# Kernel optimization log

Hardware: AMD Instinct MI355X
Metric: run time of the kernel (lower is better)

The kernel has to match this reference:

```python
import jax, jax.numpy as jnp
import numpy as np

B, S, D = 4, 2048, 1024
H, HD = 16, 64
L = 512          # kv latent dim (MLA compression)
E, TOPK, F = 8, 2, 2048  # MoE experts / top-k / expert hidden
EPS = 1e-6


def rmsnorm(x, g):
    return x * jax.lax.rsqrt(jnp.mean(x * x, axis=-1, keepdims=True) + EPS) * g


def setup_inputs() -> dict:
    key = jax.random.key(0)
    ks = jax.random.split(key, 16)
    std = 0.02
    inp = {
        "prev_hidden": jax.random.normal(ks[0], (B, S, D), jnp.float32),
        "future_token_embed": jax.random.normal(ks[1], (B, S, D), jnp.float32),
        "w_combine": jax.random.normal(ks[2], (2 * D, D), jnp.float32) * std,
        "g1": jnp.ones((D,), jnp.float32),
        "g2": jnp.ones((D,), jnp.float32),
        "g_attn": jnp.ones((D,), jnp.float32),
        "g_mlp": jnp.ones((D,), jnp.float32),
        "wq": jax.random.normal(ks[3], (D, D), jnp.float32) * std,
        "w_dkv": jax.random.normal(ks[4], (D, L), jnp.float32) * std,
        "w_uk": jax.random.normal(ks[5], (L, D), jnp.float32) * std,
        "w_uv": jax.random.normal(ks[6], (L, D), jnp.float32) * std,
        "wo": jax.random.normal(ks[7], (D, D), jnp.float32) * std,
        "w_gate": jax.random.normal(ks[8], (D, E), jnp.float32) * std,
        "w1": jax.random.normal(ks[9], (E, D, F), jnp.float32) * std,
        "w3": jax.random.normal(ks[10], (E, D, F), jnp.float32) * std,
        "w2": jax.random.normal(ks[11], (E, F, D), jnp.float32) * std,
    }
    return inp


def mla_attention(x, wq, w_dkv, w_uk, w_uv, wo):
    # Multi-head latent attention: KV compressed through latent dim L.
    q = (x @ wq).reshape(B, S, H, HD)
    c = x @ w_dkv                       # [B,S,L] latent
    k = (c @ w_uk).reshape(B, S, H, HD)
    v = (c @ w_uv).reshape(B, S, H, HD)
    scores = jnp.einsum("bqhd,bkhd->bhqk", q, k) / jnp.sqrt(jnp.float32(HD))
    causal = jnp.tril(jnp.ones((S, S), bool))
    scores = jnp.where(causal, scores, jnp.float32(-1e9))
    attn = jax.nn.softmax(scores, axis=-1)
    out = jnp.einsum("bhqk,bkhd->bqhd", attn, v).reshape(B, S, D)
    return out @ wo


def moe(x, w_gate, w1, w3, w2):
    t = x.reshape(-1, D)                          # [T,D]
    probs = jax.nn.softmax(t @ w_gate, axis=-1)   # [T,E]
    vals, idx = jax.lax.top_k(probs, TOPK)        # [T,K]
    vals = vals / jnp.sum(vals, axis=-1, keepdims=True)
    gates = jnp.sum(vals[:, :, None] * jax.nn.one_hot(idx, E, dtype=x.dtype), axis=1)  # [T,E]
    out = jnp.zeros_like(t)
    for e in range(E):  # fixed small expert loop (structurally distinct weights)
        h = jax.nn.silu(t @ w1[e]) * (t @ w3[e])
        out = out + gates[:, e:e + 1] * (h @ w2[e])
    return out.reshape(x.shape)


def reference(prev_hidden, future_token_embed, w_combine, g1, g2, g_attn, g_mlp,
              wq, w_dkv, w_uk, w_uv, wo, w_gate, w1, w3, w2):
    prev_norm = rmsnorm(prev_hidden, g1)
    future_norm = rmsnorm(future_token_embed, g2)
    combined = jnp.concatenate([prev_norm, future_norm], axis=-1)
    hidden = combined @ w_combine
    hidden = hidden + mla_attention(rmsnorm(hidden, g_attn), wq, w_dkv, w_uk, w_uv, wo)
    hidden = hidden + moe(rmsnorm(hidden, g_mlp), w_gate, w1, w3, w2)
    return hidden
```

## Files before the change

### kernel.cpp

```cpp
#include <hip/hip_runtime.h>
#include <hip/hip_bf16.h>
#include <stdint.h>

#define B_ 4
#define S_ 2048
#define D_ 1024
#define H_ 16
#define L_ 512
#define E_ 8
#define F_ 2048
#define T_ (B_*S_)

typedef __hip_bfloat16 bf16_t;
typedef __attribute__((ext_vector_type(8))) short short8;
typedef __attribute__((ext_vector_type(4))) float f32x4;

__device__ __forceinline__ void gl2lds16(const void* g, void* l) {
  __builtin_amdgcn_global_load_lds(
      reinterpret_cast<const __attribute__((address_space(1))) void*>(reinterpret_cast<uintptr_t>(g)),
      reinterpret_cast<__attribute__((address_space(3))) void*>(reinterpret_cast<uintptr_t>(l)),
      16, 0, 0);
}
__device__ __forceinline__ unsigned short bf16u(bf16_t b) {
  return *reinterpret_cast<unsigned short*>(&b);
}
__device__ __forceinline__ void split2(float v, bf16_t& ho, bf16_t& lo) {
  ho = __float2bfloat16(v);
  lo = __float2bfloat16(v - __bfloat162float(ho));
}
__device__ __forceinline__ float bf2f(bf16_t b) { return __bfloat162float(b); }

__global__ __launch_bounds__(256) void k_fill(float* out, float code, int n) {
  int i = blockIdx.x * 256 + threadIdx.x;
  if (i < n) out[i] = (i == 0 ? code : 0.f);
}

__global__ __launch_bounds__(256) void k_transpose(const float* __restrict__ in,
                                                   bf16_t* __restrict__ out, int R, int C, int ldin,
                                                   size_t zin, size_t zout) {
  __shared__ float t[32][33];
  const float* inz = in + (size_t)blockIdx.z * zin;
  bf16_t* outz = out + (size_t)blockIdx.z * zout;
  int c0 = blockIdx.x * 32, r0 = blockIdx.y * 32;
  int tx = threadIdx.x, ty = threadIdx.y;
#pragma unroll
  for (int i = 0; i < 4; ++i)
    t[ty + 8*i][tx] = inz[(size_t)(r0 + ty + 8*i) * ldin + c0 + tx];
  __syncthreads();
#pragma unroll
  for (int i = 0; i < 4; ++i)
    outz[(size_t)(c0 + ty + 8*i) * R + r0 + tx] = __float2bfloat16(t[tx][ty + 8*i]);
}

__global__ __launch_bounds__(256) void k_transpose2(const float* __restrict__ in,
                                                    bf16_t* __restrict__ oh, bf16_t* __restrict__ ol,
                                                    int R, int C, int ldin) {
  __shared__ float t[32][33];
  int c0 = blockIdx.x * 32, r0 = blockIdx.y * 32;
  int tx = threadIdx.x, ty = threadIdx.y;
#pragma unroll
  for (int i = 0; i < 4; ++i)
    t[ty + 8*i][tx] = in[(size_t)(r0 + ty + 8*i) * ldin + c0 + tx];
  __syncthreads();
#pragma unroll
  for (int i = 0; i < 4; ++i) {
    float v = t[tx][ty + 8*i];
    size_t idx = (size_t)(c0 + ty + 8*i) * R + r0 + tx;
    bf16_t h, l; split2(v, h, l);
    oh[idx] = h; ol[idx] = l;
  }
}

__global__ __launch_bounds__(256) void k_rms2cat2(const float* __restrict__ pa, const float* __restrict__ pb,
                                                  const float* __restrict__ g1, const float* __restrict__ g2,
                                                  bf16_t* __restrict__ oh, bf16_t* __restrict__ ol) {
  const int row = blockIdx.x, tid = threadIdx.x;
  float4 a = reinterpret_cast<const float4*>(pa + (size_t)row * D_)[tid];
  float4 b = reinterpret_cast<const float4*>(pb + (size_t)row * D_)[tid];
  float sa = a.x*a.x + a.y*a.y + a.z*a.z + a.w*a.w;
  float sb = b.x*b.x + b.y*b.y + b.z*b.z + b.w*b.w;
#pragma unroll
  for (int o = 32; o; o >>= 1) { sa += __shfl_xor(sa, o, 64); sb += __shfl_xor(sb, o, 64); }
  __shared__ float red[8];
  if ((tid & 63) == 0) { red[tid >> 6] = sa; red[4 + (tid >> 6)] = sb; }
  __syncthreads();
  sa = red[0] + red[1] + red[2] + red[3];
  sb = red[4] + red[5] + red[6] + red[7];
  float ra = rsqrtf(sa * (1.f / D_) + 1e-6f);
  float rb = rsqrtf(sb * (1.f / D_) + 1e-6f);
  float4 ga = reinterpret_cast<const float4*>(g1)[tid];
  float4 gb = reinterpret_cast<const float4*>(g2)[tid];
  float va[4] = {a.x*ra*ga.x, a.y*ra*ga.y, a.z*ra*ga.z, a.w*ra*ga.w};
  float vb[4] = {b.x*rb*gb.x, b.y*rb*gb.y, b.z*rb*gb.z, b.w*rb*gb.w};
  size_t base = (size_t)row * 2 * D_ + tid * 4;
#pragma unroll
  for (int j = 0; j < 4; ++j) {
    bf16_t h, l;
    split2(va[j], h, l); oh[base + j] = h; ol[base + j] = l;
    split2(vb[j], h, l); oh[base + D_ + j] = h; ol[base + D_ + j] = l;
  }
}

template <bool LO>
__global__ __launch_bounds__(256) void k_rmsnorm2(const float* __restrict__ x, const float* __restrict__ g,
                                                  bf16_t* __restrict__ oh, bf16_t* __restrict__ ol) {
  const int row = blockIdx.x, tid = threadIdx.x;
  float4 v = reinterpret_cast<const float4*>(x + (size_t)row * D_)[tid];
  float ss = v.x*v.x + v.y*v.y + v.z*v.z + v.w*v.w;
#pragma unroll
  for (int o = 32; o; o >>= 1) ss += __shfl_xor(ss, o, 64);
  __shared__ float red[4];
  if ((tid & 63) == 0) red[tid >> 6] = ss;
  __syncthreads();
  ss = red[0] + red[1] + red[2] + red[3];
  float rs = rsqrtf(ss * (1.f / D_) + 1e-6f);
  float4 gv = reinterpret_cast<const float4*>(g)[tid];
  float y[4] = {v.x*rs*gv.x, v.y*rs*gv.y, v.z*rs*gv.z, v.w*rs*gv.w};
  size_t base = (size_t)row * D_ + tid * 4;
#pragma unroll
  for (int j = 0; j < 4; ++j) {
    bf16_t h, l; split2(y[j], h, l);
    oh[base + j] = h;
    if constexpr (LO) ol[base + j] = l;
  }
}

__global__ __launch_bounds__(64) void k_gate(const float* __restrict__ hid, const float* __restrict__ gm,
                                             const float* __restrict__ wg, float* __restrict__ gates) {
  const int t = blockIdx.x, l = threadIdx.x;
  const float* xr = hid + (size_t)t * D_;
  float xv[16];
  float ss = 0.f;
#pragma unroll
  for (int i = 0; i < 16; ++i) { float x = xr[l + 64 * i]; xv[i] = x; ss += x * x; }
#pragma unroll
  for (int o = 32; o; o >>= 1) ss += __shfl_xor(ss, o, 64);
  float rs = rsqrtf(ss * (1.f / D_) + 1e-6f);
  float acc[8] = {0, 0, 0, 0, 0, 0, 0, 0};
#pragma unroll
  for (int i = 0; i < 16; ++i) {
    int d = l + 64 * i;
    float xf = xv[i] * rs * gm[d];
#pragma unroll
    for (int e = 0; e < 8; ++e) acc[e] += xf * wg[d * 8 + e];
  }
#pragma unroll
  for (int e = 0; e < 8; ++e) {
#pragma unroll
    for (int o = 32; o; o >>= 1) acc[e] += __shfl_xor(acc[e], o, 64);
  }
  float mx = acc[0];
#pragma unroll
  for (int e = 1; e < 8; ++e) mx = fmaxf(mx, acc[e]);
  float p[8], sum = 0.f;
#pragma unroll
  for (int e = 0; e < 8; ++e) { p[e] = __expf(acc[e] - mx); sum += p[e]; }
#pragma unroll
  for (int e = 0; e < 8; ++e) p[e] /= sum;
  int i0 = 0; float v0 = p[0];
#pragma unroll
  for (int e = 1; e < 8; ++e) if (p[e] > v0) { v0 = p[e]; i0 = e; }
  int i1 = -1; float v1 = -1.f;
#pragma unroll
  for (int e = 0; e < 8; ++e) if (e != i0 && p[e] > v1) { v1 = p[e]; i1 = e; }
  float norm = v0 + v1;
  if (l < 8) gates[(size_t)t * 8 + l] = (l == i0) ? v0 / norm : ((l == i1) ? v1 / norm : 0.f);
}

__global__ __launch_bounds__(256) void k_route_det(const float* __restrict__ gates,
                                                   int* __restrict__ idx, int* __restrict__ cnt) {
  const int e = blockIdx.x, tid = threadIdx.x;
  __shared__ int sc[256];
  int base = 0;
  for (int c0 = 0; c0 < T_; c0 += 256) {
    int t = c0 + tid;
    int m = (gates[(size_t)t * 8 + e] > 0.f) ? 1 : 0;
    sc[tid] = m;
    __syncthreads();
#pragma unroll
    for (int off = 1; off < 256; off <<= 1) {
      int v = (tid >= off) ? sc[tid - off] : 0;
      __syncthreads();
      sc[tid] += v;
      __syncthreads();
    }
    if (m) idx[e * T_ + base + sc[tid] - 1] = t;
    int tot = sc[255];
    __syncthreads();
    base += tot;
  }
  if (tid == 0) cnt[e] = base;
}

__global__ void k_prefix(const int* __restrict__ cnt, int* __restrict__ off) {
  int s = 0;
  for (int e = 0; e < E_; ++e) { off[e] = s; s += cnt[e]; }
}

template <int EPI, int SPLIT, int IDX>
__global__ __launch_bounds__(256) void k_sgemm(
    const bf16_t* __restrict__ Ah, const bf16_t* __restrict__ Al,
    const bf16_t* __restrict__ Bh, const bf16_t* __restrict__ Bl,
    float* __restrict__ Cf, bf16_t* __restrict__ Cb, bf16_t* __restrict__ Cb2,
    bf16_t* __restrict__ Cb3, bf16_t* __restrict__ Cb4,
    const float* __restrict__ scale, const int* __restrict__ aidx, const int* __restrict__ cnt,
    int N, int K, int lda, int ldc) {
  __shared__ __align__(16) char lds[(SPLIT == 3 ? 4 : 2) * 16384];
  char* lsAh = lds;
  char* lsBh = lds + 16384;
  char* lsAl = lds + 32768;
  char* lsBl = lds + 49152;
  const int tid = threadIdx.x;
  const int l = tid & 63;
  const int g16 = l >> 4, c16 = l & 15;
  const int nbn = N >> 7;
  int swz = (int)blockIdx.x;
  if constexpr (IDX == 0 && EPI != 6) {
    swz = (swz & 7) * ((int)gridDim.x >> 3) + (swz >> 3);
  }
  const int bm = swz / nbn, bn = swz % nbn;
  const int m0 = bm << 7, n0 = bn << 7;
  const int w = tid >> 6;
  const int wr = w >> 1, wc = w & 1;

  int cval = 0;
  if constexpr (IDX == 1 || EPI == 6) {
    cval = *cnt;
    if (m0 >= cval) return;
  }

  f32x4 acc[4][4] = {};

  int Lb[4], sr[4], sk[4];
#pragma unroll
  for (int i = 0; i < 4; ++i) {
    Lb[i] = (tid + i * 256) * 16;
    sr[i] = Lb[i] >> 7;
    sk[i] = ((Lb[i] & 127) ^ ((sr[i] & 7) << 4)) >> 1;
  }
  int arow[4];
#pragma unroll
  for (int i = 0; i < 4; ++i) {
    if constexpr (IDX == 1) {
      int p = m0 + sr[i];
      arow[i] = aidx[p < cval ? p : cval - 1];
    } else {
      arow[i] = m0 + sr[i];
    }
  }

  for (int k0 = 0; k0 < K; k0 += 64) {
#pragma unroll
    for (int i = 0; i < 4; ++i) {
      size_t aoff = (size_t)arow[i] * lda + k0 + sk[i];
      size_t boff = (size_t)(n0 + sr[i]) * K + k0 + sk[i];
      gl2lds16(Ah + aoff, lsAh + Lb[i]);
      gl2lds16(Bh + boff, lsBh + Lb[i]);
      if constexpr (SPLIT == 3) {
        gl2lds16(Al + aoff, lsAl + Lb[i]);
        gl2lds16(Bl + boff, lsBl + Lb[i]);
      }
    }
    __syncthreads();
#pragma unroll
    for (int kc = 0; kc < 2; ++kc) {
      const int kb = (kc * 32 + 8 * g16) * 2;
      short8 afh[4], bfh[4], afl[4], bfl[4];
#pragma unroll
      for (int m = 0; m < 4; ++m) {
        int row = wr * 64 + m * 16 + c16;
        int off = row * 128 + (kb ^ ((row & 7) << 4));
        afh[m] = *reinterpret_cast<const short8*>(lsAh + off);
        if constexpr (SPLIT == 3) afl[m] = *reinterpret_cast<const short8*>(lsAl + off);
      }
#pragma unroll
      for (int n = 0; n < 4; ++n) {
        int row = wc * 64 + n * 16 + c16;
        int off = row * 128 + (kb ^ ((row & 7) << 4));
        bfh[n] = *reinterpret_cast<const short8*>(lsBh + off);
        if constexpr (SPLIT == 3) bfl[n] = *reinterpret_cast<const short8*>(lsBl + off);
      }
#pragma unroll
      for (int m = 0; m < 4; ++m)
#pragma unroll
        for (int n = 0; n < 4; ++n) {
          if constexpr (SPLIT == 3) {
            acc[m][n] = __builtin_amdgcn_mfma_f32_16x16x32_bf16(afl[m], bfh[n], acc[m][n], 0, 0, 0);
            acc[m][n] = __builtin_amdgcn_mfma_f32_16x16x32_bf16(afh[m], bfl[n], acc[m][n], 0, 0, 0);
          }
          acc[m][n] = __builtin_amdgcn_mfma_f32_16x16x32_bf16(afh[m], bfh[n], acc[m][n], 0, 0, 0);
        }
    }
    __syncthreads();
  }

#pragma unroll
  for (int m = 0; m < 4; ++m) {
    int rb = m0 + wr * 64 + m * 16 + 4 * g16;
#pragma unroll
    for (int n = 0; n < 4; ++n) {
      int gc = n0 + wc * 64 + n * 16 + c16;
#pragma unroll
      for (int r = 0; r < 4; ++r) {
        float v = acc[m][n][r];
        if constexpr (EPI == 6) {
          int rbr = rb + r;
          if (rbr < cval) {
            int tok = aidx[rbr];
            Cf[(size_t)tok * ldc + gc] += scale[(size_t)tok * 8] * v;
          }
        } else if constexpr (EPI == 7) {
          int t = rb + r;
          bf16_t h, lo; split2(v, h, lo);
          if (gc < 1024) {
            size_t ki = (size_t)t * 1024 + gc;
            Cb[ki] = h; Cb2[ki] = lo;
          } else {
            size_t vi = (size_t)(t >> 11) * 2097152 + (size_t)(gc - 1024) * 2048 + (t & 2047);
            Cb3[vi] = h; Cb4[vi] = lo;
          }
        } else {
          size_t idx = (size_t)(rb + r) * ldc + gc;
          if constexpr (EPI == 0) Cf[idx] = v;
          if constexpr (EPI == 1) Cf[idx] += v;
          if constexpr (EPI == 2) { bf16_t h, lo; split2(v, h, lo); Cb[idx] = h; Cb2[idx] = lo; }
          if constexpr (EPI == 3) Cb[idx] = __float2bfloat16(v / (1.f + __expf(-v)));
          if constexpr (EPI == 4) Cb[idx] = __float2bfloat16(bf2f(Cb[idx]) * v);
        }
      }
    }
  }
}

__global__ __launch_bounds__(256) void k_moe1(
    const bf16_t* __restrict__ xn, const bf16_t* __restrict__ w1t, const bf16_t* __restrict__ w3t,
    bf16_t* __restrict__ hg, const int* __restrict__ idx8, const int* __restrict__ cnt8,
    const int* __restrict__ off8) {
  __shared__ __align__(16) char lds[3 * 16384];
  char* lsA = lds;
  char* lsB1 = lds + 16384;
  char* lsB2 = lds + 32768;
  const int tid = threadIdx.x, l = tid & 63, g16 = l >> 4, c16 = l & 15;
  const int e = blockIdx.z;
  const int nbn = F_ >> 7;
  const int bm = (int)blockIdx.x / nbn, bn = (int)blockIdx.x % nbn;
  const int m0 = bm << 7, n0 = bn << 7;
  const int w = tid >> 6, wr = w >> 1, wc = w & 1;
  const int* aidx = idx8 + e * T_;
  const int cval = cnt8[e];
  if (m0 >= cval) return;
  const int obase = off8[e];
  const bf16_t* B1 = w1t + (size_t)e * D_ * F_;
  const bf16_t* B2 = w3t + (size_t)e * D_ * F_;

  f32x4 a1[4][4] = {}, a3[4][4] = {};
  int Lb[4], sr[4], sk[4], arow[4];
#pragma unroll
  for (int i = 0; i < 4; ++i) {
    Lb[i] = (tid + i * 256) * 16;
    sr[i] = Lb[i] >> 7;
    sk[i] = ((Lb[i] & 127) ^ ((sr[i] & 7) << 4)) >> 1;
    int p = m0 + sr[i];
    arow[i] = aidx[p < cval ? p : cval - 1];
  }
  for (int k0 = 0; k0 < D_; k0 += 64) {
#pragma unroll
    for (int i = 0; i < 4; ++i) {
      gl2lds16(xn + (size_t)arow[i] * D_ + k0 + sk[i], lsA + Lb[i]);
      size_t boff = (size_t)(n0 + sr[i]) * D_ + k0 + sk[i];
      gl2lds16(B1 + boff, lsB1 + Lb[i]);
      gl2lds16(B2 + boff, lsB2 + Lb[i]);
    }
    __syncthreads();
#pragma unroll
    for (int kc = 0; kc < 2; ++kc) {
      const int kb = (kc * 32 + 8 * g16) * 2;
      short8 af[4], b1[4], b2[4];
#pragma unroll
      for (int m = 0; m < 4; ++m) {
        int row = wr * 64 + m * 16 + c16;
        af[m] = *reinterpret_cast<const short8*>(lsA + row * 128 + (kb ^ ((row & 7) << 4)));
      }
#pragma unroll
      for (int n = 0; n < 4; ++n) {
        int row = wc * 64 + n * 16 + c16;
        int off = row * 128 + (kb ^ ((row & 7) << 4));
        b1[n] = *reinterpret_cast<const short8*>(lsB1 + off);
        b2[n] = *reinterpret_cast<const short8*>(lsB2 + off);
      }
#pragma unroll
      for (int m = 0; m < 4; ++m)
#pragma unroll
        for (int n = 0; n < 4; ++n) {
          a1[m][n] = __builtin_amdgcn_mfma_f32_16x16x32_bf16(af[m], b1[n], a1[m][n], 0, 0, 0);
          a3[m][n] = __builtin_amdgcn_mfma_f32_16x16x32_bf16(af[m], b2[n], a3[m][n], 0, 0, 0);
        }
    }
    __syncthreads();
  }
#pragma unroll
  for (int m = 0; m < 4; ++m) {
    int rb = m0 + wr * 64 + m * 16 + 4 * g16;
#pragma unroll
    for (int n = 0; n < 4; ++n) {
      int gc = n0 + wc * 64 + n * 16 + c16;
#pragma unroll
      for (int r = 0; r < 4; ++r) {
        int rbr = rb + r;
        if (rbr < cval) {
          float v1 = a1[m][n][r], v3 = a3[m][n][r];
          hg[(size_t)(obase + rbr) * F_ + gc] = __float2bfloat16(v1 / (1.f + __expf(-v1)) * v3);
        }
      }
    }
  }
}

__global__ __launch_bounds__(256) void k_moe2z(
    const bf16_t* __restrict__ hg, const bf16_t* __restrict__ w2t,
    float* __restrict__ hid, const float* __restrict__ gates,
    const int* __restrict__ idx8, const int* __restrict__ cnt8, const int* __restrict__ off8) {
  __shared__ __align__(16) char lds[2 * 16384];
  char* lsA = lds;
  char* lsB = lds + 16384;
  const int tid = threadIdx.x, l = tid & 63, g16 = l >> 4, c16 = l & 15;
  const int e = blockIdx.z;
  const int nbn = D_ >> 7;
  const int bm = (int)blockIdx.x / nbn, bn = (int)blockIdx.x % nbn;
  const int m0 = bm << 7, n0 = bn << 7;
  const int w = tid >> 6, wr = w >> 1, wc = w & 1;
  const int* aidx = idx8 + e * T_;
  const int cval = cnt8[e];
  if (m0 >= cval) return;
  const int obase = off8[e];
  const bf16_t* Bt = w2t + (size_t)e * D_ * F_;

  f32x4 acc[4][4] = {};
  int Lb[4], sr[4], sk[4];
#pragma unroll
  for (int i = 0; i < 4; ++i) {
    Lb[i] = (tid + i * 256) * 16;
    sr[i] = Lb[i] >> 7;
    sk[i] = ((Lb[i] & 127) ^ ((sr[i] & 7) << 4)) >> 1;
  }
  for (int k0 = 0; k0 < F_; k0 += 64) {
#pragma unroll
    for (int i = 0; i < 4; ++i) {
      gl2lds16(hg + (size_t)(obase + m0 + sr[i]) * F_ + k0 + sk[i], lsA + Lb[i]);
      gl2lds16(Bt + (size_t)(n0 + sr[i]) * F_ + k0 + sk[i], lsB + Lb[i]);
    }
    __syncthreads();
#pragma unroll
    for (int kc = 0; kc < 2; ++kc) {
      const int kb = (kc * 32 + 8 * g16) * 2;
      short8 af[4], bf8[4];
#pragma unroll
      for (int m = 0; m < 4; ++m) {
        int row = wr * 64 + m * 16 + c16;
        af[m] = *reinterpret_cast<const short8*>(lsA + row * 128 + (kb ^ ((row & 7) << 4)));
      }
#pragma unroll
      for (int n = 0; n < 4; ++n) {
        int row = wc * 64 + n * 16 + c16;
        bf8[n] = *reinterpret_cast<const short8*>(lsB + row * 128 + (kb ^ ((row & 7) << 4)));
      }
#pragma unroll
      for (int m = 0; m < 4; ++m)
#pragma unroll
        for (int n = 0; n < 4; ++n)
          acc[m][n] = __builtin_amdgcn_mfma_f32_16x16x32_bf16(af[m], bf8[n], acc[m][n], 0, 0, 0);
    }
    __syncthreads();
  }
#pragma unroll
  for (int m = 0; m < 4; ++m) {
    int rb = m0 + wr * 64 + m * 16 + 4 * g16;
#pragma unroll
    for (int n = 0; n < 4; ++n) {
      int gc = n0 + wc * 64 + n * 16 + c16;
#pragma unroll
      for (int r = 0; r < 4; ++r) {
        int rbr = rb + r;
        if (rbr < cval) {
          int tok = aidx[rbr];
          atomicAdd(&hid[(size_t)tok * D_ + gc], gates[(size_t)tok * 8 + e] * acc[m][n][r]);
        }
      }
    }
  }
}

__global__ __launch_bounds__(512) void k_flash8(
    const bf16_t* __restrict__ qh, const bf16_t* __restrict__ ql,
    const bf16_t* __restrict__ kbh, const bf16_t* __restrict__ kbl,
    const bf16_t* __restrict__ vth, const bf16_t* __restrict__ vtl,
    bf16_t* __restrict__ ch, bf16_t* __restrict__ cl, int zb) {
  __shared__ __align__(16) char lds[98304];
  const int tid = threadIdx.x, l = tid & 63, w = tid >> 6;
  const int g16 = l >> 4, c16 = l & 15;
  const int qt = (int)gridDim.y - 1 - (int)blockIdx.y;
  const int h = (int)blockIdx.x / zb;
  const int z = (int)blockIdx.x % zb;
  const int zS = z * S_;
  const size_t vz = (size_t)z * 2097152;

  const int qrow = qt * 128 + w * 16 + c16;
  const size_t qoff = (size_t)(zS + qrow) * 1536 + h * 64 + 8 * g16;
  const short8 aq0h = *reinterpret_cast<const short8*>(qh + qoff);
  const short8 aq1h = *reinterpret_cast<const short8*>(qh + qoff + 32);
  const short8 aq0l = *reinterpret_cast<const short8*>(ql + qoff);
  const short8 aq1l = *reinterpret_cast<const short8*>(ql + qoff + 32);

  float mrow[4] = {-3e38f, -3e38f, -3e38f, -3e38f};
  float lrow[4] = {0.f, 0.f, 0.f, 0.f};
  f32x4 o[4] = {};
  char* Pwh = lds + 65536 + w * 2048;
  char* Pwl = lds + 81920 + w * 2048;

  auto stage = [&](int buf, int kt) {
    char* base = lds + buf * 32768;
    int Lb = tid * 16;
    int r = Lb >> 7;
    int dd = ((Lb & 127) ^ ((r & 7) << 4)) >> 1;
    size_t ko = (size_t)(zS + kt * 64 + r) * 1024 + h * 64 + dd;
    size_t vo = vz + (size_t)(h * 64 + r) * 2048 + kt * 64 + dd;
    gl2lds16(kbh + ko, base + Lb);
    gl2lds16(kbl + ko, base + 8192 + Lb);
    gl2lds16(vth + vo, base + 16384 + Lb);
    gl2lds16(vtl + vo, base + 24576 + Lb);
  };

  const int nkt = 2 * qt + 2;
  stage(0, 0);
  for (int kt = 0; kt < nkt; ++kt) {
    const int cb = kt & 1;
    char* Kh = lds + cb * 32768;
    char* Kl = Kh + 8192;
    char* Vh = Kh + 16384;
    char* Vl = Kh + 24576;
    __syncthreads();
    if (kt + 1 < nkt) stage(cb ^ 1, kt + 1);

    f32x4 s[4] = {};
#pragma unroll
    for (int kc = 0; kc < 2; ++kc) {
      const short8 ah8 = kc ? aq1h : aq0h;
      const short8 al8 = kc ? aq1l : aq0l;
      const int kb = (kc * 32 + 8 * g16) * 2;
#pragma unroll
      for (int n = 0; n < 4; ++n) {
        int row = n * 16 + c16;
        int off = row * 128 + (kb ^ ((row & 7) << 4));
        short8 bkh = *reinterpret_cast<const short8*>(Kh + off);
        short8 bkl = *reinterpret_cast<const short8*>(Kl + off);
        s[n] = __builtin_amdgcn_mfma_f32_16x16x32_bf16(al8, bkh, s[n], 0, 0, 0);
        s[n] = __builtin_amdgcn_mfma_f32_16x16x32_bf16(ah8, bkl, s[n], 0, 0, 0);
        s[n] = __builtin_amdgcn_mfma_f32_16x16x32_bf16(ah8, bkh, s[n], 0, 0, 0);
      }
    }

    const bool dreg = (kt >= 2 * qt);
#pragma unroll
    for (int r = 0; r < 4; ++r) {
      const int rowabs = qt * 128 + w * 16 + 4 * g16 + r;
      float mx = -3e38f;
#pragma unroll
      for (int n = 0; n < 4; ++n) {
        float sv = s[n][r] * 0.125f;
        if (dreg && (kt * 64 + n * 16 + c16 > rowabs)) sv = -3e38f;
        s[n][r] = sv;
        mx = fmaxf(mx, sv);
      }
      mx = fmaxf(mx, __shfl_xor(mx, 1, 64));
      mx = fmaxf(mx, __shfl_xor(mx, 2, 64));
      mx = fmaxf(mx, __shfl_xor(mx, 4, 64));
      mx = fmaxf(mx, __shfl_xor(mx, 8, 64));
      float mnew = fmaxf(mrow[r], mx);
      float alpha = __expf(mrow[r] - mnew);
      float rsum = 0.f;
#pragma unroll
      for (int n = 0; n < 4; ++n) {
        float pp = __expf(s[n][r] - mnew);
        s[n][r] = pp;
        rsum += pp;
      }
      rsum += __shfl_xor(rsum, 1, 64);
      rsum += __shfl_xor(rsum, 2, 64);
      rsum += __shfl_xor(rsum, 4, 64);
      rsum += __shfl_xor(rsum, 8, 64);
      lrow[r] = lrow[r] * alpha + rsum;
      mrow[r] = mnew;
#pragma unroll
      for (int n = 0; n < 4; ++n) o[n][r] *= alpha;
    }

#pragma unroll
    for (int n = 0; n < 4; ++n)
#pragma unroll
      for (int r = 0; r < 4; ++r) {
        int row = 4 * g16 + r, col = n * 16 + c16;
        int off = row * 128 + ((col * 2) ^ ((row & 7) << 4));
        bf16_t ph, pl; split2(s[n][r], ph, pl);
        *reinterpret_cast<unsigned short*>(Pwh + off) = bf16u(ph);
        *reinterpret_cast<unsigned short*>(Pwl + off) = bf16u(pl);
      }

#pragma unroll
    for (int kc = 0; kc < 2; ++kc) {
      const int kb = (kc * 32 + 8 * g16) * 2;
      int poff = c16 * 128 + (kb ^ ((c16 & 7) << 4));
      short8 aph = *reinterpret_cast<const short8*>(Pwh + poff);
      short8 apl = *reinterpret_cast<const short8*>(Pwl + poff);
#pragma unroll
      for (int n = 0; n < 4; ++n) {
        int dr = n * 16 + c16;
        int off = dr * 128 + (kb ^ ((dr & 7) << 4));
        short8 bvh = *reinterpret_cast<const short8*>(Vh + off);
        short8 bvl = *reinterpret_cast<const short8*>(Vl + off);
        o[n] = __builtin_amdgcn_mfma_f32_16x16x32_bf16(apl, bvh, o[n], 0, 0, 0);
        o[n] = __builtin_amdgcn_mfma_f32_16x16x32_bf16(aph, bvl, o[n], 0, 0, 0);
        o[n] = __builtin_amdgcn_mfma_f32_16x16x32_bf16(aph, bvh, o[n], 0, 0, 0);
      }
    }
  }

#pragma unroll
  for (int n = 0; n < 4; ++n)
#pragma unroll
    for (int r = 0; r < 4; ++r) {
      float val = o[n][r] / lrow[r];
      size_t idx = (size_t)(zS + qt * 128 + w * 16 + 4 * g16 + r) * 1024 + h * 64 + n * 16 + c16;
      bf16_t hh, ll; split2(val, hh, ll);
      ch[idx] = hh; cl[idx] = ll;
    }
}

extern "C" void kernel_launch(void* const* d_in, const int* in_sizes, int n_in,
                              void* d_out, int out_size, void* d_ws, size_t ws_size,
                              hipStream_t stream) {
  const size_t MB = 1ull << 20;

  static const int dictSz[16] = {8388608, 8388608, 2097152, 1024, 1024, 1024, 1024,
                                 1048576, 524288, 524288, 524288, 1048576, 8192,
                                 16777216, 16777216, 16777216};
  static const int alphaSz[16] = {8388608, 1024, 1024, 1024, 1024, 8388608,
                                  16777216, 16777216, 16777216, 2097152, 524288,
                                  8192, 524288, 524288, 1048576, 1048576};
  bool isDict = (n_in == 16), isAlpha = (n_in == 16);
  for (int i = 0; i < 16; ++i) {
    if (n_in != 16) break;
    if (in_sizes[i] != dictSz[i]) isDict = false;
    if (in_sizes[i] != alphaSz[i]) isAlpha = false;
  }
  if ((!isDict && !isAlpha) || ws_size < 64 * MB) {
    k_fill<<<(out_size + 255) / 256, 256, 0, stream>>>((float*)d_out, 444.f, out_size);
    return;
  }

  const float *prev, *fut, *w_combine, *g1, *g2, *g_attn, *g_mlp, *wq, *w_dkv,
      *w_uk, *w_uv, *wo, *w_gate, *w1, *w3, *w2;
  if (isDict) {
    prev = (const float*)d_in[0];  fut = (const float*)d_in[1];
    w_combine = (const float*)d_in[2];
    g1 = (const float*)d_in[3];  g2 = (const float*)d_in[4];
    g_attn = (const float*)d_in[5];  g_mlp = (const float*)d_in[6];
    wq = (const float*)d_in[7];  w_dkv = (const float*)d_in[8];
    w_uk = (const float*)d_in[9];  w_uv = (const float*)d_in[10];
    wo = (const float*)d_in[11];  w_gate = (const float*)d_in[12];
    w1 = (const float*)d_in[13];  w3 = (const float*)d_in[14];
    w2 = (const float*)d_in[15];
  } else {
    fut = (const float*)d_in[0];
    g1 = (const float*)d_in[1];  g2 = (const float*)d_in[2];
    g_attn = (const float*)d_in[3];  g_mlp = (const float*)d_in[4];
    prev = (const float*)d_in[5];
    w1 = (const float*)d_in[6];  w2 = (const float*)d_in[7];  w3 = (const float*)d_in[8];
    w_combine = (const float*)d_in[9];  w_dkv = (const float*)d_in[10];
    w_gate = (const float*)d_in[11];  w_uk = (const float*)d_in[12];
    w_uv = (const float*)d_in[13];  wo = (const float*)d_in[14];
    wq = (const float*)d_in[15];
  }

  float* hid = (float*)d_out;
  char* ws = (char*)d_ws;
  const bool big = (ws_size >= 192 * MB);

  bf16_t* wcth = (bf16_t*)(ws + 0 * MB);
  bf16_t* wctl = (bf16_t*)(ws + 4 * MB);
  bf16_t* qcTh = (bf16_t*)(ws + 0 * MB);
  bf16_t* qcTl = (bf16_t*)(ws + 3 * MB);
  bf16_t* kvTh = (bf16_t*)(ws + 6 * MB);
  bf16_t* kvTl = (bf16_t*)(ws + 8 * MB);
  bf16_t* woth = (bf16_t*)(ws + 10 * MB);
  bf16_t* wotl = (bf16_t*)(ws + 12 * MB);
  bf16_t* w1t  = (bf16_t*)(ws + 0 * MB);
  bf16_t* w3t  = (bf16_t*)(ws + 4 * MB);
  bf16_t* w2t  = (bf16_t*)(ws + 8 * MB);
  float*  gates = (float*)(ws + 14 * MB);
  int*    idx   = (int*)(ws + 14 * MB + 262144);
  int*    cnt   = (int*)(ws + 14 * MB + 524288);
  int*    off   = (int*)(ws + 14 * MB + 524288 + 64);
  bf16_t* xnh = (bf16_t*)(ws + 15 * MB);

  dim3 tb(32, 8);

  if (big) {
    bf16_t* xcath = (bf16_t*)(ws + 15 * MB);
    bf16_t* xcatl = (bf16_t*)(ws + 47 * MB);
    bf16_t* xnbh  = (bf16_t*)(ws + 15 * MB);
    bf16_t* xnbl  = (bf16_t*)(ws + 31 * MB);
    bf16_t* qch   = (bf16_t*)(ws + 47 * MB);
    bf16_t* qcl   = (bf16_t*)(ws + 71 * MB);
    bf16_t* kbh   = (bf16_t*)(ws + 95 * MB);
    bf16_t* kbl   = (bf16_t*)(ws + 111 * MB);
    bf16_t* vth   = (bf16_t*)(ws + 127 * MB);
    bf16_t* vtl   = (bf16_t*)(ws + 143 * MB);
    bf16_t* ctxh  = (bf16_t*)(ws + 159 * MB);
    bf16_t* ctxl  = (bf16_t*)(ws + 175 * MB);
    bf16_t* hg    = (bf16_t*)(ws + 31 * MB);
    bf16_t* w1tA  = (bf16_t*)(ws + 95 * MB);
    bf16_t* w3tA  = (bf16_t*)(ws + 127 * MB);
    bf16_t* w2tA  = (bf16_t*)(ws + 159 * MB);

    k_transpose2<<<dim3(32, 64), tb, 0, stream>>>(w_combine, wcth, wctl, 2 * D_, D_, D_);
    k_rms2cat2<<<T_, 256, 0, stream>>>(prev, fut, g1, g2, xcath, xcatl);
    k_sgemm<0, 3, 0><<<dim3(64 * 8), 256, 0, stream>>>(
        xcath, xcatl, wcth, wctl, hid, nullptr, nullptr, nullptr, nullptr,
        nullptr, nullptr, nullptr, D_, 2 * D_, 2 * D_, D_);

    k_transpose2<<<dim3(32, 32), tb, 0, stream>>>(wq, qcTh, qcTl, D_, D_, D_);
    k_transpose2<<<dim3(16, 32), tb, 0, stream>>>(w_dkv, qcTh + 1024 * 1024, qcTl + 1024 * 1024, D_, L_, L_);
    k_transpose2<<<dim3(32, 16), tb, 0, stream>>>(w_uk, kvTh, kvTl, L_, D_, D_);
    k_transpose2<<<dim3(32, 16), tb, 0, stream>>>(w_uv, kvTh + 1024 * 512, kvTl + 1024 * 512, L_, D_, D_);
    k_transpose2<<<dim3(32, 32), tb, 0, stream>>>(wo, woth, wotl, D_, D_, D_);
    k_rmsnorm2<true><<<T_, 256, 0, stream>>>(hid, g_attn, xnbh, xnbl);
    k_sgemm<2, 3, 0><<<dim3(64 * 12), 256, 0, stream>>>(
        xnbh, xnbl, qcTh, qcTl, nullptr, qch, qcl, nullptr, nullptr,
        nullptr, nullptr, nullptr, 1536, D_, D_, 1536);
    k_sgemm<7, 3, 0><<<dim3(64 * 16), 256, 0, stream>>>(
        qch + 1024, qcl + 1024, kvTh, kvTl, nullptr, kbh, kbl, vth, vtl,
        nullptr, nullptr, nullptr, 2048, L_, 1536, 1024);
    k_flash8<<<dim3(H_ * B_, 16, 1), 512, 0, stream>>>(qch, qcl, kbh, kbl, vth, vtl, ctxh, ctxl, B_);
    k_sgemm<1, 3, 0><<<dim3(64 * 8), 256, 0, stream>>>(
        ctxh, ctxl, woth, wotl, hid, nullptr, nullptr, nullptr, nullptr,
        nullptr, nullptr, nullptr, D_, D_, D_, D_);

    k_rmsnorm2<false><<<T_, 256, 0, stream>>>(hid, g_mlp, xnh, nullptr);
    k_gate<<<T_, 64, 0, stream>>>(hid, g_mlp, w_gate, gates);
    k_route_det<<<E_, 256, 0, stream>>>(gates, idx, cnt);
    k_prefix<<<1, 1, 0, stream>>>(cnt, off);
    k_transpose<<<dim3(64, 32, 8), tb, 0, stream>>>(w1, w1tA, D_, F_, F_, (size_t)D_ * F_, (size_t)F_ * D_);
    k_transpose<<<dim3(64, 32, 8), tb, 0, stream>>>(w3, w3tA, D_, F_, F_, (size_t)D_ * F_, (size_t)F_ * D_);
    k_transpose<<<dim3(32, 64, 8), tb, 0, stream>>>(w2, w2tA, F_, D_, D_, (size_t)F_ * D_, (size_t)D_ * F_);
    k_moe1<<<dim3(64 * 16, 1, 8), 256, 0, stream>>>(xnh, w1tA, w3tA, hg, idx, cnt, off);
    k_moe2z<<<dim3(64 * 8, 1, 8), 256, 0, stream>>>(hg, w2tA, hid, gates, idx, cnt, off);
  } else {
    bf16_t* xcath = (bf16_t*)(ws + 15 * MB);
    bf16_t* xcatl = (bf16_t*)(ws + 23 * MB);
    bf16_t* xnbh  = (bf16_t*)(ws + 15 * MB);
    bf16_t* xnbl  = (bf16_t*)(ws + 19 * MB);
    bf16_t* qch   = (bf16_t*)(ws + 23 * MB);
    bf16_t* qcl   = (bf16_t*)(ws + 29 * MB);
    bf16_t* kbh   = (bf16_t*)(ws + 35 * MB);
    bf16_t* kbl   = (bf16_t*)(ws + 39 * MB);
    bf16_t* vth   = (bf16_t*)(ws + 43 * MB);
    bf16_t* vtl   = (bf16_t*)(ws + 47 * MB);
    bf16_t* ctxh  = (bf16_t*)(ws + 51 * MB);
    bf16_t* ctxl  = (bf16_t*)(ws + 55 * MB);
    bf16_t* hg    = (bf16_t*)(ws + 31 * MB);

    k_transpose2<<<dim3(32, 64), tb, 0, stream>>>(w_combine, wcth, wctl, 2 * D_, D_, D_);
    for (int b = 0; b < B_; ++b) {
      size_t ro = (size_t)b * S_ * D_;
      k_rms2cat2<<<S_, 256, 0, stream>>>(prev + ro, fut + ro, g1, g2, xcath, xcatl);
      k_sgemm<0, 3, 0><<<dim3(16 * 8), 256, 0, stream>>>(
          xcath, xcatl, wcth, wctl, hid + ro, nullptr, nullptr, nullptr, nullptr,
          nullptr, nullptr, nullptr, D_, 2 * D_, 2 * D_, D_);
    }
    k_transpose2<<<dim3(32, 32), tb, 0, stream>>>(wq, qcTh, qcTl, D_, D_, D_);
    k_transpose2<<<dim3(16, 32), tb, 0, stream>>>(w_dkv, qcTh + 1024 * 1024, qcTl + 1024 * 1024, D_, L_, L_);
    k_transpose2<<<dim3(32, 16), tb, 0, stream>>>(w_uk, kvTh, kvTl, L_, D_, D_);
    k_transpose2<<<dim3(32, 16), tb, 0, stream>>>(w_uv, kvTh + 1024 * 512, kvTl + 1024 * 512, L_, D_, D_);
    k_transpose2<<<dim3(32, 32), tb, 0, stream>>>(wo, woth, wotl, D_, D_, D_);
    for (int b = 0; b < B_; ++b) {
      size_t ro = (size_t)b * S_ * D_;
      k_rmsnorm2<true><<<S_, 256, 0, stream>>>(hid + ro, g_attn, xnbh, xnbl);
      k_sgemm<2, 3, 0><<<dim3(16 * 12), 256, 0, stream>>>(
          xnbh, xnbl, qcTh, qcTl, nullptr, qch, qcl, nullptr, nullptr,
          nullptr, nullptr, nullptr, 1536, D_, D_, 1536);
      k_sgemm<7, 3, 0><<<dim3(16 * 16), 256, 0, stream>>>(
          qch + 1024, qcl + 1024, kvTh, kvTl, nullptr, kbh, kbl, vth, vtl,
          nullptr, nullptr, nullptr, 2048, L_, 1536, 1024);
      k_flash8<<<dim3(H_, 16, 1), 512, 0, stream>>>(qch, qcl, kbh, kbl, vth, vtl, ctxh, ctxl, 1);
      k_sgemm<1, 3, 0><<<dim3(16 * 8), 256, 0, stream>>>(
          ctxh, ctxl, woth, wotl, hid + ro, nullptr, nullptr, nullptr, nullptr,
          nullptr, nullptr, nullptr, D_, D_, D_, D_);
    }
    k_rmsnorm2<false><<<T_, 256, 0, stream>>>(hid, g_mlp, xnh, nullptr);
    k_gate<<<T_, 64, 0, stream>>>(hid, g_mlp, w_gate, gates);
    k_route_det<<<E_, 256, 0, stream>>>(gates, idx, cnt);
    for (int e = 0; e < E_; ++e) {
      const int* ide = idx + e * T_;
      const int* cne = cnt + e;
      k_transpose<<<dim3(64, 32, 1), tb, 0, stream>>>(w1 + (size_t)e * D_ * F_, w1t, D_, F_, F_, 0, 0);
      k_transpose<<<dim3(64, 32, 1), tb, 0, stream>>>(w3 + (size_t)e * D_ * F_, w3t, D_, F_, F_, 0, 0);
      k_transpose<<<dim3(32, 64, 1), tb, 0, stream>>>(w2 + (size_t)e * F_ * D_, w2t, F_, D_, D_, 0, 0);
      k_sgemm<3, 1, 1><<<dim3(64 * 16), 256, 0, stream>>>(
          xnh, nullptr, w1t, nullptr, nullptr, hg, nullptr, nullptr, nullptr,
          nullptr, ide, cne, F_, D_, D_, F_);
      k_sgemm<4, 1, 1><<<dim3(64 * 16), 256, 0, stream>>>(
          xnh, nullptr, w3t, nullptr, nullptr, hg, nullptr, nullptr, nullptr,
          nullptr, ide, cne, F_, D_, D_, F_);
      k_sgemm<6, 1, 0><<<dim3(64 * 8), 256, 0, stream>>>(
          hg, nullptr, w2t, nullptr, hid, nullptr, nullptr, nullptr, nullptr,
          gates + e, ide, cne, D_, F_, F_, D_);
    }
  }
}
```

Baseline: 1.288 ms.

## Widen flash attention to 256-row query tiles and fuse MLP rmsnorm with gating

```diff
diff --git a/kernel.cpp b/kernel.cpp
--- a/kernel.cpp
+++ b/kernel.cpp
@@ -101,7 +101,6 @@
   }
 }
 
-template <bool LO>
 __global__ __launch_bounds__(256) void k_rmsnorm2(const float* __restrict__ x, const float* __restrict__ g,
                                                   bf16_t* __restrict__ oh, bf16_t* __restrict__ ol) {
   const int row = blockIdx.x, tid = threadIdx.x;
@@ -121,50 +120,69 @@
   for (int j = 0; j < 4; ++j) {
     bf16_t h, l; split2(y[j], h, l);
     oh[base + j] = h;
-    if constexpr (LO) ol[base + j] = l;
-  }
-}
-
-__global__ __launch_bounds__(64) void k_gate(const float* __restrict__ hid, const float* __restrict__ gm,
-                                             const float* __restrict__ wg, float* __restrict__ gates) {
-  const int t = blockIdx.x, l = threadIdx.x;
-  const float* xr = hid + (size_t)t * D_;
-  float xv[16];
-  float ss = 0.f;
-#pragma unroll
-  for (int i = 0; i < 16; ++i) { float x = xr[l + 64 * i]; xv[i] = x; ss += x * x; }
+    ol[base + j] = l;
+  }
+}
+
+__global__ __launch_bounds__(256) void k_rmsgate(const float* __restrict__ x, const float* __restrict__ g,
+                                                 const float* __restrict__ wg,
+                                                 bf16_t* __restrict__ oh, float* __restrict__ gates) {
+  const int row = blockIdx.x, tid = threadIdx.x;
+  float4 v = reinterpret_cast<const float4*>(x + (size_t)row * D_)[tid];
+  float ss = v.x*v.x + v.y*v.y + v.z*v.z + v.w*v.w;
 #pragma unroll
   for (int o = 32; o; o >>= 1) ss += __shfl_xor(ss, o, 64);
+  __shared__ float red[4];
+  __shared__ float eacc[4][8];
+  if ((tid & 63) == 0) red[tid >> 6] = ss;
+  __syncthreads();
+  ss = red[0] + red[1] + red[2] + red[3];
   float rs = rsqrtf(ss * (1.f / D_) + 1e-6f);
+  float4 gv = reinterpret_cast<const float4*>(g)[tid];
+  float y[4] = {v.x*rs*gv.x, v.y*rs*gv.y, v.z*rs*gv.z, v.w*rs*gv.w};
+  size_t base = (size_t)row * D_ + tid * 4;
+#pragma unroll
+  for (int j = 0; j < 4; ++j) oh[base + j] = __float2bfloat16(y[j]);
   float acc[8] = {0, 0, 0, 0, 0, 0, 0, 0};
 #pragma unroll
-  for (int i = 0; i < 16; ++i) {
-    int d = l + 64 * i;
-    float xf = xv[i] * rs * gm[d];
-#pragma unroll
-    for (int e = 0; e < 8; ++e) acc[e] += xf * wg[d * 8 + e];
+  for (int j = 0; j < 4; ++j) {
+    const float* wgr = wg + (size_t)(tid * 4 + j) * 8;
+#pragma unroll
+    for (int e = 0; e < 8; ++e) acc[e] += y[j] * wgr[e];
   }
 #pragma unroll
   for (int e = 0; e < 8; ++e) {
 #pragma unroll
     for (int o = 32; o; o >>= 1) acc[e] += __shfl_xor(acc[e], o, 64);
   }
-  float mx = acc[0];
-#pragma unroll
-  for (int e = 1; e < 8; ++e) mx = fmaxf(mx, acc[e]);
-  float p[8], sum = 0.f;
-#pragma unroll
-  for (int e = 0; e < 8; ++e) { p[e] = __expf(acc[e] - mx); sum += p[e]; }
-#pragma unroll
-  for (int e = 0; e < 8; ++e) p[e] /= sum;
-  int i0 = 0; float v0 = p[0];
-#pragma unroll
-  for (int e = 1; e < 8; ++e) if (p[e] > v0) { v0 = p[e]; i0 = e; }
-  int i1 = -1; float v1 = -1.f;
-#pragma unroll
-  for (int e = 0; e < 8; ++e) if (e != i0 && p[e] > v1) { v1 = p[e]; i1 = e; }
-  float norm = v0 + v1;
-  if (l < 8) gates[(size_t)t * 8 + l] = (l == i0) ? v0 / norm : ((l == i1) ? v1 / norm : 0.f);
+  if ((tid & 63) == 0) {
+#pragma unroll
+    for (int e = 0; e < 8; ++e) eacc[tid >> 6][e] = acc[e];
+  }
+  __syncthreads();
+  if (tid == 0) {
+    float a[8];
+#pragma unroll
+    for (int e = 0; e < 8; ++e) a[e] = eacc[0][e] + eacc[1][e] + eacc[2][e] + eacc[3][e];
+    float mx = a[0];
+#pragma unroll
+    for (int e = 1; e < 8; ++e) mx = fmaxf(mx, a[e]);
+    float p[8], sum = 0.f;
+#pragma unroll
+    for (int e = 0; e < 8; ++e) { p[e] = __expf(a[e] - mx); sum += p[e]; }
+#pragma unroll
+    for (int e = 0; e < 8; ++e) p[e] /= sum;
+    int i0 = 0; float v0 = p[0];
+#pragma unroll
+    for (int e = 1; e < 8; ++e) if (p[e] > v0) { v0 = p[e]; i0 = e; }
+    int i1 = -1; float v1 = -1.f;
+#pragma unroll
+    for (int e = 0; e < 8; ++e) if (e != i0 && p[e] > v1) { v1 = p[e]; i1 = e; }
+    float norm = v0 + v1;
+#pragma unroll
+    for (int e = 0; e < 8; ++e)
+      gates[(size_t)row * 8 + e] = (e == i0) ? v0 / norm : ((e == i1) ? v1 / norm : 0.f);
+  }
 }
 
 __global__ __launch_bounds__(256) void k_route_det(const float* __restrict__ gates,
@@ -490,12 +508,12 @@
   }
 }
 
-__global__ __launch_bounds__(512) void k_flash8(
+__global__ __launch_bounds__(1024) void k_flash16(
     const bf16_t* __restrict__ qh, const bf16_t* __restrict__ ql,
     const bf16_t* __restrict__ kbh, const bf16_t* __restrict__ kbl,
     const bf16_t* __restrict__ vth, const bf16_t* __restrict__ vtl,
     bf16_t* __restrict__ ch, bf16_t* __restrict__ cl, int zb) {
-  __shared__ __align__(16) char lds[98304];
+  __shared__ __align__(16) char lds[131072];
   const int tid = threadIdx.x, l = tid & 63, w = tid >> 6;
   const int g16 = l >> 4, c16 = l & 15;
   const int qt = (int)gridDim.y - 1 - (int)blockIdx.y;
@@ -504,7 +522,7 @@
   const int zS = z * S_;
   const size_t vz = (size_t)z * 2097152;
 
-  const int qrow = qt * 128 + w * 16 + c16;
+  const int qrow = qt * 256 + w * 16 + c16;
   const size_t qoff = (size_t)(zS + qrow) * 1536 + h * 64 + 8 * g16;
   const short8 aq0h = *reinterpret_cast<const short8*>(qh + qoff);
   const short8 aq1h = *reinterpret_cast<const short8*>(qh + qoff + 32);
@@ -515,22 +533,26 @@
   float lrow[4] = {0.f, 0.f, 0.f, 0.f};
   f32x4 o[4] = {};
   char* Pwh = lds + 65536 + w * 2048;
-  char* Pwl = lds + 81920 + w * 2048;
+  char* Pwl = lds + 98304 + w * 2048;
 
   auto stage = [&](int buf, int kt) {
     char* base = lds + buf * 32768;
-    int Lb = tid * 16;
+    int t2 = tid & 511;
+    int Lb = t2 * 16;
     int r = Lb >> 7;
     int dd = ((Lb & 127) ^ ((r & 7) << 4)) >> 1;
-    size_t ko = (size_t)(zS + kt * 64 + r) * 1024 + h * 64 + dd;
-    size_t vo = vz + (size_t)(h * 64 + r) * 2048 + kt * 64 + dd;
-    gl2lds16(kbh + ko, base + Lb);
-    gl2lds16(kbl + ko, base + 8192 + Lb);
-    gl2lds16(vth + vo, base + 16384 + Lb);
-    gl2lds16(vtl + vo, base + 24576 + Lb);
+    if (tid < 512) {
+      size_t ko = (size_t)(zS + kt * 64 + r) * 1024 + h * 64 + dd;
+      gl2lds16(kbh + ko, base + Lb);
+      gl2lds16(kbl + ko, base + 8192 + Lb);
+    } else {
+      size_t vo = vz + (size_t)(h * 64 + r) * 2048 + kt * 64 + dd;
+      gl2lds16(vth + vo, base + 16384 + Lb);
+      gl2lds16(vtl + vo, base + 24576 + Lb);
+    }
   };
 
-  const int nkt = 2 * qt + 2;
+  const int nkt = 4 * qt + 4;
   stage(0, 0);
   for (int kt = 0; kt < nkt; ++kt) {
     const int cb = kt & 1;
@@ -559,10 +581,10 @@
       }
     }
 
-    const bool dreg = (kt >= 2 * qt);
+    const bool dreg = (kt >= 4 * qt);
 #pragma unroll
     for (int r = 0; r < 4; ++r) {
-      const int rowabs = qt * 128 + w * 16 + 4 * g16 + r;
+      const int rowabs = qt * 256 + w * 16 + 4 * g16 + r;
       float mx = -3e38f;
 #pragma unroll
       for (int n = 0; n < 4; ++n) {
@@ -629,7 +651,7 @@
 #pragma unroll
     for (int r = 0; r < 4; ++r) {
       float val = o[n][r] / lrow[r];
-      size_t idx = (size_t)(zS + qt * 128 + w * 16 + 4 * g16 + r) * 1024 + h * 64 + n * 16 + c16;
+      size_t idx = (size_t)(zS + qt * 256 + w * 16 + 4 * g16 + r) * 1024 + h * 64 + n * 16 + c16;
       bf16_t hh, ll; split2(val, hh, ll);
       ch[idx] = hh; cl[idx] = ll;
     }
@@ -733,20 +755,19 @@
     k_transpose2<<<dim3(32, 16), tb, 0, stream>>>(w_uk, kvTh, kvTl, L_, D_, D_);
     k_transpose2<<<dim3(32, 16), tb, 0, stream>>>(w_uv, kvTh + 1024 * 512, kvTl + 1024 * 512, L_, D_, D_);
     k_transpose2<<<dim3(32, 32), tb, 0, stream>>>(wo, woth, wotl, D_, D_, D_);
-    k_rmsnorm2<true><<<T_, 256, 0, stream>>>(hid, g_attn, xnbh, xnbl);
+    k_rmsnorm2<<<T_, 256, 0, stream>>>(hid, g_attn, xnbh, xnbl);
     k_sgemm<2, 3, 0><<<dim3(64 * 12), 256, 0, stream>>>(
         xnbh, xnbl, qcTh, qcTl, nullptr, qch, qcl, nullptr, nullptr,
         nullptr, nullptr, nullptr, 1536, D_, D_, 1536);
     k_sgemm<7, 3, 0><<<dim3(64 * 16), 256, 0, stream>>>(
         qch + 1024, qcl + 1024, kvTh, kvTl, nullptr, kbh, kbl, vth, vtl,
         nullptr, nullptr, nullptr, 2048, L_, 1536, 1024);
-    k_flash8<<<dim3(H_ * B_, 16, 1), 512, 0, stream>>>(qch, qcl, kbh, kbl, vth, vtl, ctxh, ctxl, B_);
+    k_flash16<<<dim3(H_ * B_, 8, 1), 1024, 0, stream>>>(qch, qcl, kbh, kbl, vth, vtl, ctxh, ctxl, B_);
     k_sgemm<1, 3, 0><<<dim3(64 * 8), 256, 0, stream>>>(
         ctxh, ctxl, woth, wotl, hid, nullptr, nullptr, nullptr, nullptr,
         nullptr, nullptr, nullptr, D_, D_, D_, D_);
 
-    k_rmsnorm2<false><<<T_, 256, 0, stream>>>(hid, g_mlp, xnh, nullptr);
-    k_gate<<<T_, 64, 0, stream>>>(hid, g_mlp, w_gate, gates);
+    k_rmsgate<<<T_, 256, 0, stream>>>(hid, g_mlp, w_gate, xnh, gates);
     k_route_det<<<E_, 256, 0, stream>>>(gates, idx, cnt);
     k_prefix<<<1, 1, 0, stream>>>(cnt, off);
     k_transpose<<<dim3(64, 32, 8), tb, 0, stream>>>(w1, w1tA, D_, F_, F_, (size_t)D_ * F_, (size_t)F_ * D_);
@@ -784,21 +805,21 @@
     k_transpose2<<<dim3(32, 32), tb, 0, stream>>>(wo, woth, wotl, D_, D_, D_);
     for (int b = 0; b < B_; ++b) {
       size_t ro = (size_t)b * S_ * D_;
-      k_rmsnorm2<true><<<S_, 256, 0, stream>>>(hid + ro, g_attn, xnbh, xnbl);
+      k_rmsnorm2<<<S_, 256, 0, stream>>>(hid + ro, g_attn, xnbh, xnbl);
       k_sgemm<2, 3, 0><<<dim3(16 * 12), 256, 0, stream>>>(
           xnbh, xnbl, qcTh, qcTl, nullptr, qch, qcl, nullptr, nullptr,
           nullptr, nullptr, nullptr, 1536, D_, D_, 1536);
       k_sgemm<7, 3, 0><<<dim3(16 * 16), 256, 0, stream>>>(
           qch + 1024, qcl + 1024, kvTh, kvTl, nullptr, kbh, kbl, vth, vtl,
           nullptr, nullptr, nullptr, 2048, L_, 1536, 1024);
-      k_flash8<<<dim3(H_, 16, 1), 512, 0, stream>>>(qch, qcl, kbh, kbl, vth, vtl, ctxh, ctxl, 1);
+      k_flash16<<<dim3(H_, 8, 1), 1024, 0, stream>>>(qch, qcl, kbh, kbl, vth, vtl, ctxh, ctxl, 1);
       k_sgemm<1, 3, 0><<<dim3(16 * 8), 256, 0, stream>>>(
           ctxh, ctxl, woth, wotl, hid + ro, nullptr, nullptr, nullptr, nullptr,
           nullptr, nullptr, nullptr, D_, D_, D_, D_);
     }
-    k_rmsnorm2<false><<<T_, 256, 0, stream>>>(hid, g_mlp, xnh, nullptr);
-    k_gate<<<T_, 64, 0, stream>>>(hid, g_mlp, w_gate, gates);
+    k_rmsgate<<<T_, 256, 0, stream>>>(hid, g_mlp, w_gate, xnh, gates);
     k_route_det<<<E_, 256, 0, stream>>>(gates, idx, cnt);
+    k_prefix<<<1, 1, 0, stream>>>(cnt, off);
     for (int e = 0; e < E_; ++e) {
       const int* ide = idx + e * T_;
       const int* cne = cnt + e;
```

Measured after the change: 1.293 ms. About the same (+0.4%).
